# Optimization experiments

Hardware: AMD Instinct MI355X
Metric: run time of the kernel (lower is better)

Reference implementation:

```python
import jax, jax.numpy as jnp
import numpy as np

D_MODEL = 1024
N_HEADS = 16
HEAD_DIM = D_MODEL // N_HEADS
B, SQ, SK = 2, 2048, 2048


def setup_inputs() -> dict:
    key = jax.random.key(0)
    ks = jax.random.split(key, 12)
    init = 0.02
    inp = {
        "queries": jax.random.normal(ks[0], (B, SQ, D_MODEL), jnp.float32),
        "keys": jax.random.normal(ks[1], (B, SK, D_MODEL), jnp.float32),
        "values": jax.random.normal(ks[2], (B, SK, D_MODEL), jnp.float32),
        "Wq": jax.random.normal(ks[3], (D_MODEL, D_MODEL), jnp.float32) * init,
        "bq": jnp.zeros((D_MODEL,), jnp.float32),
        "Wk": jax.random.normal(ks[4], (D_MODEL, D_MODEL), jnp.float32) * init,
        "bk": jnp.zeros((D_MODEL,), jnp.float32),
        "Wv": jax.random.normal(ks[5], (D_MODEL, D_MODEL), jnp.float32) * init,
        "bv": jnp.zeros((D_MODEL,), jnp.float32),
        "Wo": jax.random.normal(ks[6], (D_MODEL, D_MODEL), jnp.float32) * init,
        "bo": jnp.zeros((D_MODEL,), jnp.float32),
        # causal mask: True = attend (matches masked_fill(mask == False, -inf))
        "mask": jnp.tril(jnp.ones((SQ, SK), dtype=bool)),
    }
    return inp


def _split_heads(x):
    # (B, S, D) -> (B, H, S, hd)
    b, s, _ = x.shape
    return x.reshape(b, s, N_HEADS, HEAD_DIM).transpose(0, 2, 1, 3)


def reference(queries, keys, values, Wq, bq, Wk, bk, Wv, bv, Wo, bo, mask):
    q = _split_heads(queries @ Wq + bq)   # (B, H, Sq, hd)
    k = _split_heads(keys @ Wk + bk)      # (B, H, Sk, hd)
    v = _split_heads(values @ Wv + bv)    # (B, H, Sk, hd)

    scale = 1.0 / np.sqrt(HEAD_DIM).astype(np.float32)
    scores = jnp.einsum("bhqd,bhkd->bhqk", q, k) * scale
    neg = jnp.finfo(scores.dtype).min
    scores = jnp.where(mask[None, None, :, :], scores, neg)
    probs = jax.nn.softmax(scores, axis=-1)
    out = jnp.einsum("bhqk,bhkd->bhqd", probs, v)  # (B, H, Sq, hd)

    b, h, sq, hd = out.shape
    out = out.transpose(0, 2, 1, 3).reshape(b, sq, h * hd)  # combine heads
    return out @ Wo + bo
```

## Files before the change

kernel.cpp:

```cpp
#include <hip/hip_runtime.h>


typedef short bf16x8 __attribute__((ext_vector_type(8)));
typedef short bf16x4 __attribute__((ext_vector_type(4)));
typedef float f32x4 __attribute__((ext_vector_type(4)));
typedef float f32x16 __attribute__((ext_vector_type(16)));
typedef unsigned u32x4 __attribute__((ext_vector_type(4)));

#define LOG2E 1.44269504f

__device__ __forceinline__ short f2bf(float x) {
    unsigned u = __builtin_bit_cast(unsigned, x);
    u += 0x7fffu + ((u >> 16) & 1u);
    return (short)(u >> 16);
}

__device__ __forceinline__ float bf2f(short s) {
    unsigned u = ((unsigned)(unsigned short)s) << 16;
    return __builtin_bit_cast(float, u);
}

__device__ __forceinline__ float fexp2(float x) {
    float r;
    asm("v_exp_f32 %0, %1" : "=v"(r) : "v"(x));
    return r;
}

__device__ __forceinline__ unsigned cvtpk(float lo, float hi) {
    unsigned r;
    asm("v_cvt_pk_bf16_f32 %0, %1, %2" : "=v"(r) : "v"(lo), "v"(hi));
    return r;
}

__device__ __forceinline__ void gload16(const short* g, short* l) {
    __builtin_amdgcn_global_load_lds((const __attribute__((address_space(1))) void*)g,
                                     (__attribute__((address_space(3))) void*)l, 16, 0, 0);
}

__global__ __launch_bounds__(256) void cvt_x(
    const float* __restrict__ xq, const float* __restrict__ xk,
    const float* __restrict__ xv, short* __restrict__ xb)
{
    size_t g = (size_t)blockIdx.x * 256 + threadIdx.x;
    int z = (int)(g >> 19);
    size_t off = (g & 524287) * 8;
    const float* src = (z == 0) ? xq : (z == 1) ? xk : xv;
    float4 a = *(const float4*)(src + off);
    float4 b = *(const float4*)(src + off + 4);
    bf16x8 o = { f2bf(a.x), f2bf(a.y), f2bf(a.z), f2bf(a.w),
                 f2bf(b.x), f2bf(b.y), f2bf(b.z), f2bf(b.w) };
    *(bf16x8*)(xb + (size_t)z * 4194304 + off) = o;
}

__global__ __launch_bounds__(256) void cvt_w(
    const float* __restrict__ Wq, const float* __restrict__ Wk,
    const float* __restrict__ Wv, const float* __restrict__ Wo,
    short* __restrict__ wb)
{
    __shared__ short T[64][72];
    const int z = blockIdx.z;
    const float* W = (z == 0) ? Wq : (z == 1) ? Wk : (z == 2) ? Wv : Wo;
    const int k0 = blockIdx.y * 64, n0 = blockIdx.x * 64;
    const int tid = threadIdx.x;

    #pragma unroll
    for (int p = 0; p < 4; ++p) {
        int idx = p * 256 + tid;
        int r = idx >> 4, c4 = (idx & 15) * 4;
        float4 wv = *(const float4*)(W + (size_t)(k0 + r) * 1024 + n0 + c4);
        T[c4 + 0][r] = f2bf(wv.x);
        T[c4 + 1][r] = f2bf(wv.y);
        T[c4 + 2][r] = f2bf(wv.z);
        T[c4 + 3][r] = f2bf(wv.w);
    }
    __syncthreads();
    #pragma unroll
    for (int p = 0; p < 2; ++p) {
        int idx = p * 256 + tid;
        int n = idx >> 3, c8 = (idx & 7) * 8;
        *(bf16x8*)(wb + (size_t)z * 1048576 + (size_t)(n0 + n) * 1024 + k0 + c8) =
            *(const bf16x8*)(&T[n][c8]);
    }
}

#define GEMM_CORE(A_, Bt_, ACC_)                                                         \
    const short* srcA[4]; const short* srcB[4]; short* dstA[4]; short* dstB[4];          \
    _Pragma("unroll")                                                                    \
    for (int p = 0; p < 4; ++p) {                                                        \
        int idx = p * 256 + tid;                                                         \
        int row = idx >> 3;                                                              \
        int c8 = (idx & 7) ^ (row & 7);                                                  \
        srcA[p] = (A_)  + (size_t)(m0 + row) * 1024 + c8 * 8;                            \
        srcB[p] = (Bt_) + (size_t)(n0 + row) * 1024 + c8 * 8;                            \
        dstA[p] = As + idx * 8;                                                          \
        dstB[p] = Bs + idx * 8;                                                          \
    }                                                                                    \
    for (int k0 = 0; k0 < 1024; k0 += 64) {                                              \
        __syncthreads();                                                                 \
        _Pragma("unroll")                                                                \
        for (int p = 0; p < 4; ++p) {                                                    \
            gload16(srcA[p] + k0, dstA[p]);                                              \
            gload16(srcB[p] + k0, dstB[p]);                                              \
        }                                                                                \
        __syncthreads();                                                                 \
        _Pragma("unroll")                                                                \
        for (int kf = 0; kf < 2; ++kf) {                                                 \
            bf16x8 af[4], bfr[4];                                                        \
            _Pragma("unroll")                                                            \
            for (int mi = 0; mi < 4; ++mi) {                                             \
                int row = wr + mi * 16 + lr;                                             \
                af[mi] = *(const bf16x8*)(As + row * 64 + (((kf << 2) | lh) ^ (row & 7)) * 8); \
            }                                                                            \
            _Pragma("unroll")                                                            \
            for (int ni = 0; ni < 4; ++ni) {                                             \
                int row = wc + ni * 16 + lr;                                             \
                bfr[ni] = *(const bf16x8*)(Bs + row * 64 + (((kf << 2) | lh) ^ (row & 7)) * 8); \
            }                                                                            \
            _Pragma("unroll")                                                            \
            for (int mi = 0; mi < 4; ++mi)                                               \
                _Pragma("unroll")                                                        \
                for (int ni = 0; ni < 4; ++ni)                                           \
                    ACC_[mi][ni] = __builtin_amdgcn_mfma_f32_16x16x32_bf16(af[mi], bfr[ni], ACC_[mi][ni], 0, 0, 0); \
        }                                                                                \
    }

__global__ __launch_bounds__(256, 3) void qkv_gemm(
    const short* __restrict__ xb, const short* __restrict__ wb,
    const float* __restrict__ bq, const float* __restrict__ bk, const float* __restrict__ bv,
    short* __restrict__ qpk, short* __restrict__ kpk, short* __restrict__ vpk)
{
    __shared__ short As[128 * 64];
    __shared__ short Bs[128 * 64];
    const int z = blockIdx.z;
    const short* A  = xb + (size_t)z * 4194304;
    const short* Bt = wb + (size_t)z * 1048576;
    const float* bias = (z == 0) ? bq : (z == 1) ? bk : bv;
    const float oscale = (z == 0) ? (0.125f * LOG2E) : 1.0f;

    const int tid = threadIdx.x;
    const int m0 = blockIdx.y * 128, n0 = blockIdx.x * 128;
    const int w = tid >> 6, lane = tid & 63, lr = lane & 15, lh = lane >> 4;
    const int wr = (w >> 1) * 64, wc = (w & 1) * 64;

    f32x4 acc[4][4] = {};
    GEMM_CORE(A, Bt, acc)

    #pragma unroll
    for (int ni = 0; ni < 4; ++ni) {
        int c = n0 + wc + ni * 16 + lr;
        float bv_ = bias[c];
        int hh = c >> 6, d = c & 63;
        #pragma unroll
        for (int mi = 0; mi < 4; ++mi) {
            if (z == 2) {
                int rr0 = m0 + wr + mi * 16 + lh * 4;
                int b = rr0 >> 11, ss = rr0 & 2047;
                int bh = b * 16 + hh;
                int dm = d >> 5, dr = d & 31;
                int kt = ss >> 6, ks = (ss >> 4) & 3, h2 = (ss >> 3) & 1, el0 = ss & 7;
                bf16x4 pv = { f2bf(acc[mi][ni][0] + bv_), f2bf(acc[mi][ni][1] + bv_),
                              f2bf(acc[mi][ni][2] + bv_), f2bf(acc[mi][ni][3] + bv_) };
                *(bf16x4*)(vpk + ((((size_t)bh * 32 + kt) * 2 + dm) * 4 + ks) * 512
                               + (h2 * 32 + dr) * 8 + el0) = pv;
            } else {
                #pragma unroll
                for (int j = 0; j < 4; ++j) {
                    int rr = m0 + wr + mi * 16 + lh * 4 + j;
                    int b = rr >> 11, ss = rr & 2047;
                    int bh = b * 16 + hh;
                    float val = (acc[mi][ni][j] + bv_) * oscale;
                    if (z == 0) {
                        int strip = ss >> 5, qr = ss & 31;
                        int kk = d >> 4, h2 = (d >> 3) & 1, el = d & 7;
                        qpk[(((size_t)bh * 64 + strip) * 4 + kk) * 512 + (h2 * 32 + qr) * 8 + el] = f2bf(val);
                    } else {
                        int kt = ss >> 6, m = (ss >> 5) & 1, kr = ss & 31;
                        int kk = d >> 4, h2 = (d >> 3) & 1, el = d & 7;
                        kpk[((((size_t)bh * 32 + kt) * 2 + m) * 4 + kk) * 512 + (h2 * 32 + kr) * 8 + el] = f2bf(val);
                    }
                }
            }
        }
    }
}

__global__ __launch_bounds__(256, 3) void out_gemm(
    const short* __restrict__ ao, const short* __restrict__ wbo,
    const float* __restrict__ bo, float* __restrict__ out)
{
    __shared__ short As[128 * 64];
    __shared__ short Bs[128 * 64];
    const int tid = threadIdx.x;
    const int m0 = blockIdx.y * 128, n0 = blockIdx.x * 128;
    const int w = tid >> 6, lane = tid & 63, lr = lane & 15, lh = lane >> 4;
    const int wr = (w >> 1) * 64, wc = (w & 1) * 64;

    f32x4 acc[4][4] = {};
    GEMM_CORE(ao, wbo, acc)

    #pragma unroll
    for (int ni = 0; ni < 4; ++ni) {
        int c = n0 + wc + ni * 16 + lr;
        float bv_ = bo[c];
        #pragma unroll
        for (int mi = 0; mi < 4; ++mi) {
            #pragma unroll
            for (int j = 0; j < 4; ++j) {
                int r = m0 + wr + mi * 16 + lh * 4 + j;
                out[(size_t)r * 1024 + c] = acc[mi][ni][j] + bv_;
            }
        }
    }
}


__global__ __launch_bounds__(256, 3) void attn_part(
    const short* __restrict__ qpk, const short* __restrict__ kpk,
    const short* __restrict__ vpk, short* __restrict__ opart, float2* __restrict__ ml)
{
    __shared__ short lds[2][8192];

    const int tid = threadIdx.x, w = tid >> 6, lane = tid & 63;
    const int r = lane & 31, h = lane >> 5;

    const int bid = blockIdx.x;
    const int xcd = bid & 7, jj = bid >> 3;
    const int bh = xcd * 4 + (jj & 3);
    const int u = 39 - (jj >> 2);
    int g, c;
    if (u < 4)       { g = u; c = 0; }
    else if (u < 12) { int t = u - 4;  g = 4 + (t >> 1); c = t & 1; }
    else if (u < 24) { int t = u - 12; g = 8 + t / 3;    c = t % 3; }
    else             { int t = u - 24; g = 12 + (t >> 2); c = t & 3; }

    const int s = 4 * g + w;
    const int nt_w = s / 2 + 1;
    const int ntq = 2 * g + 2;
    const int kt0 = c * 8;
    const int ktMax  = (kt0 + 8 < ntq) ? (kt0 + 8) : ntq;
    const int ktEndw = (ktMax < nt_w) ? ktMax : nt_w;
    const int q = s * 32 + r;

    const short* qbase = qpk + (((size_t)bh * 64 + s) * 4) * 512 + lane * 8;
    bf16x8 aq[4];
    #pragma unroll
    for (int kk = 0; kk < 4; ++kk) aq[kk] = *(const bf16x8*)(qbase + kk * 512);

    const short* kbh = kpk + (size_t)bh * 32 * 4096;
    const short* vbh = vpk + (size_t)bh * 32 * 4096;

#define STAGE(BUF, KT)                                                        \
    {                                                                         \
        const short* sk = kbh + (size_t)(KT) * 4096;                          \
        const short* sv = vbh + (size_t)(KT) * 4096;                          \
        short* dk = &lds[BUF][0];                                             \
        short* dv = &lds[BUF][4096];                                          \
        _Pragma("unroll")                                                     \
        for (int p = 0; p < 2; ++p)                                           \
            gload16(sk + (p * 256 + tid) * 8, dk + (p * 256 + tid) * 8);      \
        _Pragma("unroll")                                                     \
        for (int p = 0; p < 2; ++p)                                           \
            gload16(sv + (p * 256 + tid) * 8, dv + (p * 256 + tid) * 8);      \
    }

    float m_i = -1e30f, l_i = 0.0f;
    f32x16 o0 = {}, o1 = {};

    STAGE(0, kt0)
    __syncthreads();

    int buf = 0;
    for (int kt = kt0; kt < ktMax; ++kt) {
        if (kt + 1 < ktMax) STAGE(buf ^ 1, kt + 1)

        if (kt < ktEndw) {
            const short* lk = &lds[buf][0] + lane * 8;
            const short* lv = &lds[buf][4096] + lane * 8;

            f32x16 s0 = {}, s1 = {};
            #pragma unroll
            for (int kk = 0; kk < 4; ++kk) {
                bf16x8 kf = *(const bf16x8*)(lk + kk * 512);
                s0 = __builtin_amdgcn_mfma_f32_32x32x16_bf16(kf, aq[kk], s0, 0, 0, 0);
            }
            #pragma unroll
            for (int kk = 0; kk < 4; ++kk) {
                bf16x8 kf = *(const bf16x8*)(lk + (4 + kk) * 512);
                s1 = __builtin_amdgcn_mfma_f32_32x32x16_bf16(kf, aq[kk], s1, 0, 0, 0);
            }

            if (kt == nt_w - 1) {
                const int base = kt * 64 + 4 * h;
                #pragma unroll
                for (int m = 0; m < 2; ++m) {
                    f32x16& sv_ = m ? s1 : s0;
                    #pragma unroll
                    for (int p = 0; p < 16; ++p) {
                        int key = base + m * 32 + (p & 3) + 8 * (p >> 2);
                        if (key > q) sv_[p] = -1e30f;
                    }
                }
            }

            float mx[16];
            #pragma unroll
            for (int p = 0; p < 16; ++p) mx[p] = fmaxf(s0[p], s1[p]);
            #pragma unroll
            for (int st = 8; st >= 1; st >>= 1)
                #pragma unroll
                for (int p = 0; p < 16; ++p) if (p < st) mx[p] = fmaxf(mx[p], mx[p + st]);
            float v = mx[0];
            if (!__all(v <= m_i + 11.0f)) {
                float vf = fmaxf(v, __shfl_xor(v, 32));
                float mnew = fmaxf(m_i, vf);
                float corr = fexp2(m_i - mnew);
                m_i = mnew;
                l_i *= corr;
                #pragma unroll
                for (int p = 0; p < 16; ++p) { o0[p] *= corr; o1[p] *= corr; }
            }
            float ps[16];
            #pragma unroll
            for (int p = 0; p < 16; ++p) {
                s0[p] = fexp2(s0[p] - m_i);
                s1[p] = fexp2(s1[p] - m_i);
                ps[p] = s0[p] + s1[p];
            }
            #pragma unroll
            for (int st = 8; st >= 1; st >>= 1)
                #pragma unroll
                for (int p = 0; p < 16; ++p) if (p < st) ps[p] += ps[p + st];
            float psum = ps[0];
            psum += __shfl_xor(psum, 32);
            l_i += psum;

            bf16x8 pb[4];
            #pragma unroll
            for (int ks = 0; ks < 4; ++ks) {
                const f32x16& sm_ = (ks >> 1) ? s1 : s0;
                const int pb0 = (ks & 1) * 8;
                unsigned A0 = cvtpk(sm_[pb0 + 0], sm_[pb0 + 1]);
                unsigned B0 = cvtpk(sm_[pb0 + 4], sm_[pb0 + 5]);
                unsigned A1 = cvtpk(sm_[pb0 + 2], sm_[pb0 + 3]);
                unsigned B1 = cvtpk(sm_[pb0 + 6], sm_[pb0 + 7]);
                asm volatile("v_permlane32_swap_b32 %0, %1" : "+v"(A0), "+v"(B0));
                asm volatile("v_permlane32_swap_b32 %0, %1" : "+v"(A1), "+v"(B1));
                u32x4 wv = { A0, A1, B0, B1 };
                pb[ks] = __builtin_bit_cast(bf16x8, wv);
            }

            #pragma unroll
            for (int ks = 0; ks < 4; ++ks) {
                bf16x8 v0f = *(const bf16x8*)(lv + ks * 512);
                bf16x8 v1f = *(const bf16x8*)(lv + (4 + ks) * 512);
                o0 = __builtin_amdgcn_mfma_f32_32x32x16_bf16(v0f, pb[ks], o0, 0, 0, 0);
                o1 = __builtin_amdgcn_mfma_f32_32x32x16_bf16(v1f, pb[ks], o1, 0, 0, 0);
            }
        }

        __syncthreads();
        buf ^= 1;
    }
#undef STAGE

    int slot0;
    if (s < 16)      slot0 = s;
    else if (s < 32) slot0 = 16 + (s - 16) * 2;
    else if (s < 48) slot0 = 48 + (s - 32) * 3;
    else             slot0 = 96 + (s - 48) * 4;
    const size_t slotg = (size_t)bh * 160 + slot0 + c;

    short* op = opart + slotg * 2048 + (size_t)r * 64;
    #pragma unroll
    for (int dm = 0; dm < 2; ++dm) {
        const f32x16& o = dm ? o1 : o0;
        #pragma unroll
        for (int g4 = 0; g4 < 4; ++g4) {
            bf16x4 o4 = { f2bf(o[4 * g4 + 0]), f2bf(o[4 * g4 + 1]),
                          f2bf(o[4 * g4 + 2]), f2bf(o[4 * g4 + 3]) };
            *(bf16x4*)(op + dm * 32 + g4 * 8 + h * 4) = o4;
        }
    }
    if (h == 0) ml[slotg * 32 + r] = make_float2(m_i, l_i);
}

__global__ __launch_bounds__(128) void attn_combine(
    const short* __restrict__ opart, const float2* __restrict__ ml, short* __restrict__ ao)
{
    const int bid = blockIdx.x;
    const int bh = bid >> 6, s = bid & 63;
    const int nc = 1 + (s >= 16) + (s >= 32) + (s >= 48);
    int slot0;
    if (s < 16)      slot0 = s;
    else if (s < 32) slot0 = 16 + (s - 16) * 2;
    else if (s < 48) slot0 = 48 + (s - 32) * 3;
    else             slot0 = 96 + (s - 48) * 4;
    const size_t sg0 = (size_t)bh * 160 + slot0;

    const int tid = threadIdx.x;
    const int q = tid >> 2, dg = tid & 3;

    float M = -1e30f;
    #pragma unroll 4
    for (int c = 0; c < nc; ++c) M = fmaxf(M, ml[(sg0 + c) * 32 + q].x);

    float L = 0.f;
    float acc[16] = {};
    #pragma unroll 4
    for (int c = 0; c < nc; ++c) {
        float2 v = ml[(sg0 + c) * 32 + q];
        float w = fexp2(v.x - M);
        L += v.y * w;
        const short* src = opart + (sg0 + c) * 2048 + (size_t)q * 64 + dg * 16;
        bf16x8 a = *(const bf16x8*)src;
        bf16x8 b2 = *(const bf16x8*)(src + 8);
        #pragma unroll
        for (int j = 0; j < 8; ++j) {
            acc[j]     += w * bf2f(a[j]);
            acc[8 + j] += w * bf2f(b2[j]);
        }
    }
    const float rl = 1.0f / L;
    const int b = bh >> 4, hh = bh & 15;
    short* dst = ao + ((size_t)(b * 2048 + s * 32 + q)) * 1024 + hh * 64 + dg * 16;
    bf16x8 oa, ob;
    #pragma unroll
    for (int j = 0; j < 8; ++j) { oa[j] = f2bf(acc[j] * rl); ob[j] = f2bf(acc[8 + j] * rl); }
    *(bf16x8*)dst = oa;
    *(bf16x8*)(dst + 8) = ob;
}

extern "C" void kernel_launch(void* const* d_in, const int* in_sizes, int n_in,
                              void* d_out, int out_size, void* d_ws, size_t ws_size,
                              hipStream_t stream) {
    const float* queries = (const float*)d_in[0];
    const float* keys    = (const float*)d_in[1];
    const float* values  = (const float*)d_in[2];
    const float* Wq = (const float*)d_in[3];  const float* bq = (const float*)d_in[4];
    const float* Wk = (const float*)d_in[5];  const float* bk = (const float*)d_in[6];
    const float* Wv = (const float*)d_in[7];  const float* bv = (const float*)d_in[8];
    const float* Wo = (const float*)d_in[9];  const float* bo = (const float*)d_in[10];
    float* out = (float*)d_out;

    char* ws = (char*)d_ws;
    short*  xb    = (short*)(ws);
    short*  opart = (short*)(ws);
    float2* mlb   = (float2*)(ws + 20971520);
    short*  qpk   = (short*)(ws + (24u << 20));
    short*  ao    = (short*)(ws + (24u << 20));
    short*  kpk   = (short*)(ws + (32u << 20));
    short*  vpk   = (short*)(ws + (40u << 20));
    short*  wb    = (short*)(ws + (48u << 20));

    cvt_x<<<6144, 256, 0, stream>>>(queries, keys, values, xb);
    cvt_w<<<dim3(16, 16, 4), 256, 0, stream>>>(Wq, Wk, Wv, Wo, wb);
    qkv_gemm<<<dim3(8, 32, 3), 256, 0, stream>>>(xb, wb, bq, bk, bv, qpk, kpk, vpk);
    attn_part<<<1280, 256, 0, stream>>>(qpk, kpk, vpk, opart, mlb);
    attn_combine<<<2048, 128, 0, stream>>>(opart, mlb, ao);
    out_gemm<<<dim3(8, 32), 256, 0, stream>>>(ao, wb + (size_t)3 * 1048576, bo, out);
}
```

Baseline: 122.0 us.

## Triple-buffer attention K/V loads and remap GEMM blocks per XCD

Measured after the change: 115.7 us. -5.1%, faster.

```diff
diff --git a/kernel.cpp b/kernel.cpp
--- a/kernel.cpp
+++ b/kernel.cpp
@@ -131,14 +131,19 @@
 {
     __shared__ short As[128 * 64];
     __shared__ short Bs[128 * 64];
-    const int z = blockIdx.z;
+
+    const int jb = blockIdx.x, xcd = jb & 7, li = jb >> 3;
+    const int gj = xcd * 96 + li;
+    const int z = gj >> 8;
+    const int rem = gj & 255;
+    const int m0 = (rem >> 3) * 128, n0 = (rem & 7) * 128;
+
     const short* A  = xb + (size_t)z * 4194304;
     const short* Bt = wb + (size_t)z * 1048576;
     const float* bias = (z == 0) ? bq : (z == 1) ? bk : bv;
     const float oscale = (z == 0) ? (0.125f * LOG2E) : 1.0f;
 
     const int tid = threadIdx.x;
-    const int m0 = blockIdx.y * 128, n0 = blockIdx.x * 128;
     const int w = tid >> 6, lane = tid & 63, lr = lane & 15, lh = lane >> 4;
     const int wr = (w >> 1) * 64, wc = (w & 1) * 64;
 
@@ -190,8 +195,12 @@
 {
     __shared__ short As[128 * 64];
     __shared__ short Bs[128 * 64];
+
+    const int jb = blockIdx.x, xcd = jb & 7, li = jb >> 3;
+    const int gj = xcd * 32 + li;
+    const int m0 = (gj >> 3) * 128, n0 = (gj & 7) * 128;
+
     const int tid = threadIdx.x;
-    const int m0 = blockIdx.y * 128, n0 = blockIdx.x * 128;
     const int w = tid >> 6, lane = tid & 63, lr = lane & 15, lh = lane >> 4;
     const int wr = (w >> 1) * 64, wc = (w & 1) * 64;
 
@@ -218,7 +227,7 @@
     const short* __restrict__ qpk, const short* __restrict__ kpk,
     const short* __restrict__ vpk, short* __restrict__ opart, float2* __restrict__ ml)
 {
-    __shared__ short lds[2][8192];
+    __shared__ short lds[3][8192];
 
     const int tid = threadIdx.x, w = tid >> 6, lane = tid & 63;
     const int r = lane & 31, h = lane >> 5;
@@ -267,17 +276,25 @@
     f32x16 o0 = {}, o1 = {};
 
     STAGE(0, kt0)
-    __syncthreads();
-
-    int buf = 0;
+
+    int bi = 0;
     for (int kt = kt0; kt < ktMax; ++kt) {
-        if (kt + 1 < ktMax) STAGE(buf ^ 1, kt + 1)
+        const int nb = (bi == 2) ? 0 : bi + 1;
+        if (kt + 1 < ktMax) {
+            STAGE(nb, kt + 1)
+            asm volatile("s_waitcnt vmcnt(4)" ::: "memory");
+        } else {
+            asm volatile("s_waitcnt vmcnt(0)" ::: "memory");
+        }
+        __builtin_amdgcn_s_barrier();
+        __builtin_amdgcn_sched_barrier(0);
 
         if (kt < ktEndw) {
-            const short* lk = &lds[buf][0] + lane * 8;
-            const short* lv = &lds[buf][4096] + lane * 8;
+            const short* lk = &lds[bi][0] + lane * 8;
+            const short* lv = &lds[bi][4096] + lane * 8;
 
             f32x16 s0 = {}, s1 = {};
+            __builtin_amdgcn_s_setprio(1);
             #pragma unroll
             for (int kk = 0; kk < 4; ++kk) {
                 bf16x8 kf = *(const bf16x8*)(lk + kk * 512);
@@ -288,6 +305,7 @@
                 bf16x8 kf = *(const bf16x8*)(lk + (4 + kk) * 512);
                 s1 = __builtin_amdgcn_mfma_f32_32x32x16_bf16(kf, aq[kk], s1, 0, 0, 0);
             }
+            __builtin_amdgcn_s_setprio(0);
 
             if (kt == nt_w - 1) {
                 const int base = kt * 64 + 4 * h;
@@ -349,6 +367,7 @@
                 pb[ks] = __builtin_bit_cast(bf16x8, wv);
             }
 
+            __builtin_amdgcn_s_setprio(1);
             #pragma unroll
             for (int ks = 0; ks < 4; ++ks) {
                 bf16x8 v0f = *(const bf16x8*)(lv + ks * 512);
@@ -356,10 +375,10 @@
                 o0 = __builtin_amdgcn_mfma_f32_32x32x16_bf16(v0f, pb[ks], o0, 0, 0, 0);
                 o1 = __builtin_amdgcn_mfma_f32_32x32x16_bf16(v1f, pb[ks], o1, 0, 0, 0);
             }
-        }
-
-        __syncthreads();
-        buf ^= 1;
+            __builtin_amdgcn_s_setprio(0);
+        }
+
+        bi = nb;
     }
 #undef STAGE
 
@@ -454,8 +473,8 @@
 
     cvt_x<<<6144, 256, 0, stream>>>(queries, keys, values, xb);
     cvt_w<<<dim3(16, 16, 4), 256, 0, stream>>>(Wq, Wk, Wv, Wo, wb);
-    qkv_gemm<<<dim3(8, 32, 3), 256, 0, stream>>>(xb, wb, bq, bk, bv, qpk, kpk, vpk);
+    qkv_gemm<<<768, 256, 0, stream>>>(xb, wb, bq, bk, bv, qpk, kpk, vpk);
     attn_part<<<1280, 256, 0, stream>>>(qpk, kpk, vpk, opart, mlb);
     attn_combine<<<2048, 128, 0, stream>>>(opart, mlb, ao);
-    out_gemm<<<dim3(8, 32), 256, 0, stream>>>(ao, wb + (size_t)3 * 1048576, bo, out);
-}
+    out_gemm<<<256, 256, 0, stream>>>(ao, wb + (size_t)3 * 1048576, bo, out);
+}
```
